# Performance work log

Hardware: AMD Instinct MI355X
Metric: run time of the kernel (lower is better)

## Reference

```python
import jax, jax.numpy as jnp
import numpy as np

NUM_HEADS = 16
EMBED_DIM = 2048
HEAD_DIM = EMBED_DIM // NUM_HEADS        # 128
LATENT_DIM = HEAD_DIM // 4               # 32
GROUPS = HEAD_DIM // LATENT_DIM          # 4 latent sub-heads per q head
B, T = 1, 2048


def setup_inputs() -> dict:
    key = jax.random.key(0)
    ks = jax.random.split(key, 7)
    s_in = 1.0 / np.sqrt(EMBED_DIM)
    x = jax.random.normal(ks[0], (B, T, EMBED_DIM), dtype=jnp.float32)
    # torch Linear weights: [out_features, in_features]
    Wq = jax.random.normal(ks[1], (EMBED_DIM, EMBED_DIM), dtype=jnp.float32) * s_in
    Wk = jax.random.normal(ks[2], (EMBED_DIM, EMBED_DIM), dtype=jnp.float32) * s_in
    Wv = jax.random.normal(ks[3], (EMBED_DIM, EMBED_DIM), dtype=jnp.float32) * s_in
    Wlk = jax.random.normal(ks[4], (NUM_HEADS * LATENT_DIM, EMBED_DIM), dtype=jnp.float32) * s_in
    Wlv = jax.random.normal(ks[5], (NUM_HEADS * LATENT_DIM, EMBED_DIM), dtype=jnp.float32) * s_in
    Wo = jax.random.normal(ks[6], (EMBED_DIM, EMBED_DIM), dtype=jnp.float32) * s_in
    return {"x": x, "Wq": Wq, "Wk": Wk, "Wv": Wv, "Wlk": Wlk, "Wlv": Wlv, "Wo": Wo}


def reference(x, Wq, Wk, Wv, Wlk, Wlv, Wo):
    Bv, Tv, C = x.shape
    # q: [B,T,H,G,Dl]  (each head's 128-dim q split into 4 latent sub-heads)
    q = (x @ Wq.T).reshape(Bv, Tv, NUM_HEADS, GROUPS, LATENT_DIM)
    # latent k/v: [B,T,H,Dl], shared across the G sub-heads of each q head
    lk = (x @ Wlk.T).reshape(Bv, Tv, NUM_HEADS, LATENT_DIM)
    lv = (x @ Wlv.T).reshape(Bv, Tv, NUM_HEADS, LATENT_DIM)
    # k_proj / v_proj outputs are computed but unused in the original forward.
    scale = 1.0 / np.sqrt(HEAD_DIM).astype(np.float32)
    # scores: [B,H,G,T,T]
    scores = jnp.einsum('bthgd,bshd->bhgts', q, lk) * scale
    probs = jax.nn.softmax(scores, axis=-1)
    out = jnp.einsum('bhgts,bshd->bthgd', probs, lv).reshape(Bv, Tv, C)
    return out @ Wo.T
```

## Files before the change

kernel.cpp:

```cpp
#include <hip/hip_runtime.h>
#include <hip/hip_bf16.h>

typedef __bf16 bf16;
typedef __bf16 bf16x4 __attribute__((ext_vector_type(4)));
typedef __bf16 bf16x8 __attribute__((ext_vector_type(8)));
typedef float  f32x4  __attribute__((ext_vector_type(4)));

#define AS1 __attribute__((address_space(1)))
#define AS3 __attribute__((address_space(3)))

__device__ __forceinline__ void gload_lds16(const bf16* g, bf16* l) {
    __builtin_amdgcn_global_load_lds((const AS1 void*)g, (AS3 void*)l, 16, 0, 0);
}

__device__ __forceinline__ void stage8_f32(const float* s, bf16* l) {
    float4 a = *(const float4*)s;
    float4 b = *(const float4*)(s + 4);
    bf16x8 o;
    o[0] = (bf16)a.x; o[1] = (bf16)a.y; o[2] = (bf16)a.z; o[3] = (bf16)a.w;
    o[4] = (bf16)b.x; o[5] = (bf16)b.y; o[6] = (bf16)b.z; o[7] = (bf16)b.w;
    *(bf16x8*)l = o;
}

template <bool AF32, bool BF32>
__device__ __forceinline__ void gemm_core64(
    const void* __restrict__ Av, const void* __restrict__ Bv,
    int m0, int n0, int K, f32x4 (&acc)[2][4],
    int wm, int r16, int q8)
{
    constexpr int LDA = AF32 ? 40 : 32;
    constexpr int LDB = BF32 ? 40 : 32;
    __shared__ __align__(16) bf16 As[2][128 * LDA];
    __shared__ __align__(16) bf16 Bs[2][64 * LDB];

    const int tid = threadIdx.x;
    const int i0 = tid, i1 = tid + 256;
    const int rA0 = i0 >> 2, rA1 = i1 >> 2;
    const int rB  = tid >> 2;
    const int c0  = (tid & 3) * 8;
    const size_t a0 = (size_t)(m0 + rA0) * K + c0;
    const size_t a1 = (size_t)(m0 + rA1) * K + c0;
    const size_t b0 = (size_t)(n0 + rB)  * K + c0;

    auto stage = [&](int buf, int k0) {
        if constexpr (AF32) {
            stage8_f32((const float*)Av + a0 + k0, &As[buf][rA0 * LDA + c0]);
            stage8_f32((const float*)Av + a1 + k0, &As[buf][rA1 * LDA + c0]);
        } else {
            gload_lds16((const bf16*)Av + a0 + k0, &As[buf][i0 * 8]);
            gload_lds16((const bf16*)Av + a1 + k0, &As[buf][i1 * 8]);
        }
        if constexpr (BF32) {
            stage8_f32((const float*)Bv + b0 + k0, &Bs[buf][rB * LDB + c0]);
        } else {
            gload_lds16((const bf16*)Bv + b0 + k0, &Bs[buf][tid * 8]);
        }
    };

    stage(0, 0);
    __syncthreads();

    int cur = 0;
    for (int k0 = 0; k0 < K; k0 += 32) {
        if (k0 + 32 < K) stage(cur ^ 1, k0 + 32);

        bf16x8 a[2], b[4];
#pragma unroll
        for (int r = 0; r < 2; ++r)
            a[r] = *(const bf16x8*)&As[cur][(wm + r * 16 + r16) * LDA + q8 * 8];
#pragma unroll
        for (int c = 0; c < 4; ++c)
            b[c] = *(const bf16x8*)&Bs[cur][(c * 16 + r16) * LDB + q8 * 8];
#pragma unroll
        for (int r = 0; r < 2; ++r)
#pragma unroll
            for (int c = 0; c < 4; ++c)
                acc[r][c] = __builtin_amdgcn_mfma_f32_16x16x32_bf16(a[r], b[c], acc[r][c], 0, 0, 0);

        asm volatile("s_waitcnt vmcnt(0) lgkmcnt(0)" ::: "memory");
        __builtin_amdgcn_s_barrier();
        __builtin_amdgcn_sched_barrier(0);
        cur ^= 1;
    }
}

__global__ __launch_bounds__(256) void cvt5(
    const float* __restrict__ s0, const float* __restrict__ s1,
    const float* __restrict__ s2, const float* __restrict__ s3,
    const float* __restrict__ s4,
    bf16* __restrict__ d0, bf16* __restrict__ d1, bf16* __restrict__ d2,
    bf16* __restrict__ d3, bf16* __restrict__ d4)
{
    const float* S[5] = {s0, s1, s2, s3, s4};
    bf16*        D[5] = {d0, d1, d2, d3, d4};
    const int    N[5] = {4194304, 4194304, 1048576, 1048576, 4194304};
    int y = blockIdx.y;
    int base = (blockIdx.x * 256 + threadIdx.x) * 8;
    if (base >= N[y]) return;
    stage8_f32(S[y] + base, D[y] + base);
}

template <bool F32>
__global__ __launch_bounds__(256) void proj_kernel_t(
    const void* __restrict__ x, const void* __restrict__ Wq,
    const void* __restrict__ Wlk, const void* __restrict__ Wlv,
    bf16* __restrict__ Q, bf16* __restrict__ LK, bf16* __restrict__ LVt)
{
    const int bx = blockIdx.x, by = blockIdx.y;
    const int tid = threadIdx.x, lane = tid & 63, wave = tid >> 6;
    const int wm = wave * 32;
    const int r16 = lane & 15, q8 = lane >> 4;
    f32x4 acc[2][4] = {};

    const void* Bv; int n0;
    if (bx < 32)      { Bv = Wq;  n0 = bx * 64; }
    else if (bx < 40) { Bv = Wlk; n0 = (bx - 32) * 64; }
    else              { Bv = Wlv; n0 = (bx - 40) * 64; }

    gemm_core64<F32, F32>(x, Bv, by * 128, n0, 2048, acc, wm, r16, q8);

    if (bx < 40) {
        bf16* C  = (bx < 32) ? Q : LK;
        int ldc  = (bx < 32) ? 2048 : 512;
        const float sc = (bx < 32) ? 0.08838834764831845f * 1.4426950408889634f : 1.0f;
#pragma unroll
        for (int r = 0; r < 2; ++r)
#pragma unroll
            for (int c = 0; c < 4; ++c)
#pragma unroll
                for (int i = 0; i < 4; ++i) {
                    int row = by * 128 + wm + r * 16 + q8 * 4 + i;
                    int col = n0 + c * 16 + r16;
                    C[(size_t)row * ldc + col] = (bf16)(acc[r][c][i] * sc);
                }
    } else {
#pragma unroll
        for (int r = 0; r < 2; ++r)
#pragma unroll
            for (int c = 0; c < 4; ++c) {
                int hd = n0 + c * 16 + r16;
                int tb = by * 128 + wm + r * 16 + q8 * 4;
                bf16x4 pk;
#pragma unroll
                for (int i = 0; i < 4; ++i) pk[i] = (bf16)acc[r][c][i];
                *(bf16x4*)&LVt[(size_t)hd * 2048 + tb] = pk;
            }
    }
}

template <bool BF32>
__global__ __launch_bounds__(256) void out_kernel_t(
    const bf16* __restrict__ A, const void* __restrict__ Wo, float* __restrict__ C)
{
    const int tid = threadIdx.x, lane = tid & 63, wave = tid >> 6;
    const int wm = wave * 32;
    const int r16 = lane & 15, q8 = lane >> 4;
    f32x4 acc[2][4] = {};
    gemm_core64<false, BF32>(A, Wo, blockIdx.y * 128, blockIdx.x * 64, 2048, acc, wm, r16, q8);
#pragma unroll
    for (int r = 0; r < 2; ++r)
#pragma unroll
        for (int c = 0; c < 4; ++c)
#pragma unroll
            for (int i = 0; i < 4; ++i) {
                int row = blockIdx.y * 128 + wm + r * 16 + q8 * 4 + i;
                int col = blockIdx.x * 64 + c * 16 + r16;
                C[(size_t)row * 2048 + col] = acc[r][c][i];
            }
}

__global__ __launch_bounds__(256, 4) void attn6(
    const bf16* __restrict__ Q, const bf16* __restrict__ LK,
    const bf16* __restrict__ LVt, bf16* __restrict__ O)
{
    __shared__ __align__(16) bf16 Ks[2][64 * 32];
    __shared__ __align__(16) bf16 Vs[2][32 * 64];
    __shared__ __align__(16) bf16 Ps[128 * 64];

    const int tid  = threadIdx.x;
    const int lane = tid & 63;
    const int w    = tid >> 6;
    const int r16  = lane & 15;
    const int q8   = lane >> 4;
    const int hg = blockIdx.y, h = hg >> 2, g = hg & 3;
    const int t0 = blockIdx.x * 128;

    bf16x8 qb[2];
#pragma unroll
    for (int p = 0; p < 2; ++p)
        qb[p] = *(const bf16x8*)(Q + (size_t)(t0 + w * 32 + p * 16 + r16) * 2048
                                 + h * 128 + g * 32 + q8 * 8);

    const int kr = tid >> 2;
    const int kq = (tid & 3) ^ ((tid >> 3) & 3);
    const bf16* kg = LK + (size_t)kr * 512 + h * 32 + kq * 8;
    const int vd = tid >> 3;
    const int vq = (tid & 7) ^ ((tid >> 3) & 7);
    const bf16* vg = LVt + (size_t)(h * 32 + vd) * 2048 + vq * 8;

    const int ksw = (r16 >> 1) & 3;
    const int vsw = r16 & 7;

    const int pk7 = r16 & 7;
    const int ph  = q8 >> 1;
    const int plo = (q8 & 1) * 4;
    const int pb0 = ((w * 2 + 0) * 16 + r16) * 64;
    const int pb1 = ((w * 2 + 1) * 16 + r16) * 64;

    bf16x8 ones;
#pragma unroll
    for (int j = 0; j < 8; ++j) ones[j] = (bf16)1.0f;

    f32x4 o_acc[2][2] = {};
    f32x4 l_acc[2] = {};
    const f32x4 z = {0.f, 0.f, 0.f, 0.f};

    gload_lds16(kg, &Ks[0][tid * 8]);
    gload_lds16(vg, &Vs[0][tid * 8]);
    __syncthreads();

    int cur = 0;
    for (int sb = 0; sb < 2048; sb += 64) {
        if (sb + 64 < 2048) {
            gload_lds16(kg + (size_t)(sb + 64) * 512, &Ks[cur ^ 1][tid * 8]);
            gload_lds16(vg + (sb + 64),               &Vs[cur ^ 1][tid * 8]);
        }
        const bf16* ks = Ks[cur];
        const bf16* vs = Vs[cur];

        bf16x8 kb[4], vb[2][2];
#pragma unroll
        for (int c = 0; c < 4; ++c)
            kb[c] = *(const bf16x8*)&ks[(c * 16 + r16) * 32 + (q8 ^ ksw) * 8];
#pragma unroll
        for (int kk = 0; kk < 2; ++kk)
#pragma unroll
            for (int ct = 0; ct < 2; ++ct)
                vb[kk][ct] = *(const bf16x8*)&vs[(ct * 16 + r16) * 64
                                                 + (((kk * 4 + q8) ^ vsw) * 8)];

#pragma unroll
        for (int p = 0; p < 2; ++p) {
            const int pbase = p ? pb1 : pb0;
            f32x4 s[4];
            __builtin_amdgcn_s_setprio(1);
#pragma unroll
            for (int c = 0; c < 4; ++c)
                s[c] = __builtin_amdgcn_mfma_f32_16x16x32_bf16(kb[c], qb[p], z, 0, 0, 0);
            __builtin_amdgcn_s_setprio(0);
#pragma unroll
            for (int c = 0; c < 4; ++c) {
                bf16x4 pkv;
#pragma unroll
                for (int i = 0; i < 4; ++i) pkv[i] = (bf16)exp2f(s[c][i]);
                *(bf16x4*)&Ps[pbase + ((c * 2 + ph) ^ pk7) * 8 + plo] = pkv;
            }
        }

        __builtin_amdgcn_s_setprio(1);
#pragma unroll
        for (int p = 0; p < 2; ++p) {
            const int pbase = p ? pb1 : pb0;
#pragma unroll
            for (int kk = 0; kk < 2; ++kk) {
                bf16x8 ap = *(const bf16x8*)&Ps[pbase + ((kk * 4 + q8) ^ pk7) * 8];
#pragma unroll
                for (int ct = 0; ct < 2; ++ct)
                    o_acc[p][ct] = __builtin_amdgcn_mfma_f32_16x16x32_bf16(ap, vb[kk][ct], o_acc[p][ct], 0, 0, 0);
                l_acc[p] = __builtin_amdgcn_mfma_f32_16x16x32_bf16(ap, ones, l_acc[p], 0, 0, 0);
            }
        }
        __builtin_amdgcn_s_setprio(0);

        asm volatile("s_waitcnt vmcnt(0) lgkmcnt(0)" ::: "memory");
        __builtin_amdgcn_s_barrier();
        __builtin_amdgcn_sched_barrier(0);
        cur ^= 1;
    }

#pragma unroll
    for (int p = 0; p < 2; ++p)
#pragma unroll
        for (int i = 0; i < 4; ++i) {
            float inv = 1.0f / l_acc[p][i];
            int t = t0 + w * 32 + p * 16 + q8 * 4 + i;
#pragma unroll
            for (int ct = 0; ct < 2; ++ct) {
                int d = ct * 16 + r16;
                O[(size_t)t * 2048 + h * 128 + g * 32 + d] = (bf16)(o_acc[p][ct][i] * inv);
            }
        }
}

extern "C" void kernel_launch(void* const* d_in, const int* in_sizes, int n_in,
                              void* d_out, int out_size, void* d_ws, size_t ws_size,
                              hipStream_t stream) {
    const float* x   = (const float*)d_in[0];
    const float* Wq  = (const float*)d_in[1];
    const float* Wlk = (const float*)d_in[4];
    const float* Wlv = (const float*)d_in[5];
    const float* Wo  = (const float*)d_in[6];
    float* out = (float*)d_out;

    const size_t M4 = 4194304, M1 = 1048576;
    const size_t need_fast = (M1 + M1 + M4 + M4 + M1 + M1) * 2;

    if (ws_size >= need_fast) {
        bf16* xb   = (bf16*)d_out;
        bf16* Wqb  = xb + M4;
        bf16* p    = (bf16*)d_ws;
        bf16* Wlkb = p; p += M1;
        bf16* Wlvb = p; p += M1;
        bf16* Wob  = p; p += M4;
        bf16* Qp   = p; p += M4;
        bf16* LKp  = p; p += M1;
        bf16* LVt  = p;
        bf16* ATT  = Qp;

        cvt5<<<dim3(2048, 5), 256, 0, stream>>>(x, Wq, Wlk, Wlv, Wo,
                                                xb, Wqb, Wlkb, Wlvb, Wob);
        proj_kernel_t<false><<<dim3(48, 16), 256, 0, stream>>>(xb, Wqb, Wlkb, Wlvb,
                                                               Qp, LKp, LVt);
        attn6<<<dim3(16, 64), 256, 0, stream>>>(Qp, LKp, LVt, ATT);
        out_kernel_t<false><<<dim3(32, 16), 256, 0, stream>>>(ATT, Wob, out);
    } else {
        bf16* Qp  = (bf16*)d_ws;
        bf16* LKp = Qp + M4;
        bf16* LVt = LKp + M1;
        bf16* ATT = Qp;

        proj_kernel_t<true><<<dim3(48, 16), 256, 0, stream>>>(x, Wq, Wlk, Wlv,
                                                              Qp, LKp, LVt);
        attn6<<<dim3(16, 64), 256, 0, stream>>>(Qp, LKp, LVt, ATT);
        out_kernel_t<true><<<dim3(32, 16), 256, 0, stream>>>(ATT, Wo, out);
    }
}
```

Before: 284.6 us.

## Drop separate fp32-to-bf16 conversion pass; convert in GEMM staging, triple-buffer attention

The separate conversion kernel is removed, so the projection and output GEMMs now read fp32 inputs and weights directly. They convert to bf16 in registers while staging into XOR-swizzled LDS tiles with a K-step of 64, and prefetch the next tile into registers during the MFMA work. The attention kernel moves from double to triple buffering of K/V tiles with a partial vmcnt wait, so loads can run two iterations ahead. This avoids a full extra read and write of all weights and x, at the cost of heavier per-block global traffic (fp32 reads of weights repeated across blocks), more register pressure, and larger LDS use.

```diff
diff --git a/kernel.cpp b/kernel.cpp
--- a/kernel.cpp
+++ b/kernel.cpp
@@ -13,111 +13,96 @@
     __builtin_amdgcn_global_load_lds((const AS1 void*)g, (AS3 void*)l, 16, 0, 0);
 }
 
-__device__ __forceinline__ void stage8_f32(const float* s, bf16* l) {
-    float4 a = *(const float4*)s;
-    float4 b = *(const float4*)(s + 4);
+__device__ __forceinline__ bf16x8 pack8(const float4 a, const float4 b) {
     bf16x8 o;
     o[0] = (bf16)a.x; o[1] = (bf16)a.y; o[2] = (bf16)a.z; o[3] = (bf16)a.w;
     o[4] = (bf16)b.x; o[5] = (bf16)b.y; o[6] = (bf16)b.z; o[7] = (bf16)b.w;
-    *(bf16x8*)l = o;
-}
-
-template <bool AF32, bool BF32>
-__device__ __forceinline__ void gemm_core64(
-    const void* __restrict__ Av, const void* __restrict__ Bv,
-    int m0, int n0, int K, f32x4 (&acc)[2][4],
-    int wm, int r16, int q8)
-{
-    constexpr int LDA = AF32 ? 40 : 32;
-    constexpr int LDB = BF32 ? 40 : 32;
-    __shared__ __align__(16) bf16 As[2][128 * LDA];
-    __shared__ __align__(16) bf16 Bs[2][64 * LDB];
-
-    const int tid = threadIdx.x;
-    const int i0 = tid, i1 = tid + 256;
-    const int rA0 = i0 >> 2, rA1 = i1 >> 2;
-    const int rB  = tid >> 2;
-    const int c0  = (tid & 3) * 8;
-    const size_t a0 = (size_t)(m0 + rA0) * K + c0;
-    const size_t a1 = (size_t)(m0 + rA1) * K + c0;
-    const size_t b0 = (size_t)(n0 + rB)  * K + c0;
-
-    auto stage = [&](int buf, int k0) {
-        if constexpr (AF32) {
-            stage8_f32((const float*)Av + a0 + k0, &As[buf][rA0 * LDA + c0]);
-            stage8_f32((const float*)Av + a1 + k0, &As[buf][rA1 * LDA + c0]);
-        } else {
-            gload_lds16((const bf16*)Av + a0 + k0, &As[buf][i0 * 8]);
-            gload_lds16((const bf16*)Av + a1 + k0, &As[buf][i1 * 8]);
-        }
-        if constexpr (BF32) {
-            stage8_f32((const float*)Bv + b0 + k0, &Bs[buf][rB * LDB + c0]);
-        } else {
-            gload_lds16((const bf16*)Bv + b0 + k0, &Bs[buf][tid * 8]);
-        }
-    };
-
-    stage(0, 0);
-    __syncthreads();
-
-    int cur = 0;
-    for (int k0 = 0; k0 < K; k0 += 32) {
-        if (k0 + 32 < K) stage(cur ^ 1, k0 + 32);
-
-        bf16x8 a[2], b[4];
-#pragma unroll
-        for (int r = 0; r < 2; ++r)
-            a[r] = *(const bf16x8*)&As[cur][(wm + r * 16 + r16) * LDA + q8 * 8];
-#pragma unroll
-        for (int c = 0; c < 4; ++c)
-            b[c] = *(const bf16x8*)&Bs[cur][(c * 16 + r16) * LDB + q8 * 8];
-#pragma unroll
-        for (int r = 0; r < 2; ++r)
-#pragma unroll
-            for (int c = 0; c < 4; ++c)
-                acc[r][c] = __builtin_amdgcn_mfma_f32_16x16x32_bf16(a[r], b[c], acc[r][c], 0, 0, 0);
-
-        asm volatile("s_waitcnt vmcnt(0) lgkmcnt(0)" ::: "memory");
-        __builtin_amdgcn_s_barrier();
-        __builtin_amdgcn_sched_barrier(0);
-        cur ^= 1;
-    }
-}
-
-__global__ __launch_bounds__(256) void cvt5(
-    const float* __restrict__ s0, const float* __restrict__ s1,
-    const float* __restrict__ s2, const float* __restrict__ s3,
-    const float* __restrict__ s4,
-    bf16* __restrict__ d0, bf16* __restrict__ d1, bf16* __restrict__ d2,
-    bf16* __restrict__ d3, bf16* __restrict__ d4)
-{
-    const float* S[5] = {s0, s1, s2, s3, s4};
-    bf16*        D[5] = {d0, d1, d2, d3, d4};
-    const int    N[5] = {4194304, 4194304, 1048576, 1048576, 4194304};
-    int y = blockIdx.y;
-    int base = (blockIdx.x * 256 + threadIdx.x) * 8;
-    if (base >= N[y]) return;
-    stage8_f32(S[y] + base, D[y] + base);
-}
-
-template <bool F32>
-__global__ __launch_bounds__(256) void proj_kernel_t(
-    const void* __restrict__ x, const void* __restrict__ Wq,
-    const void* __restrict__ Wlk, const void* __restrict__ Wlv,
+    return o;
+}
+
+__global__ __launch_bounds__(256, 3) void proj9(
+    const float* __restrict__ x, const float* __restrict__ Wq,
+    const float* __restrict__ Wlk, const float* __restrict__ Wlv,
     bf16* __restrict__ Q, bf16* __restrict__ LK, bf16* __restrict__ LVt)
 {
+    __shared__ __align__(16) bf16 As[2][128 * 64];
+    __shared__ __align__(16) bf16 Bs[2][64 * 64];
+
     const int bx = blockIdx.x, by = blockIdx.y;
     const int tid = threadIdx.x, lane = tid & 63, wave = tid >> 6;
     const int wm = wave * 32;
     const int r16 = lane & 15, q8 = lane >> 4;
+    const int k7 = r16 & 7;
+
+    const float* Bp; int n0;
+    if (bx < 32)      { Bp = Wq;  n0 = bx * 64; }
+    else if (bx < 40) { Bp = Wlk; n0 = (bx - 32) * 64; }
+    else              { Bp = Wlv; n0 = (bx - 40) * 64; }
+
+    const int s = tid >> 3, c = tid & 7;
+    const int gqe = (c ^ (s & 7)) * 8;
+    const float* aSrc = x  + (size_t)(by * 128 + s) * 2048 + gqe;
+    const float* bSrc = Bp + (size_t)(n0 + s) * 2048 + gqe;
+
     f32x4 acc[2][4] = {};
-
-    const void* Bv; int n0;
-    if (bx < 32)      { Bv = Wq;  n0 = bx * 64; }
-    else if (bx < 40) { Bv = Wlk; n0 = (bx - 32) * 64; }
-    else              { Bv = Wlv; n0 = (bx - 40) * 64; }
-
-    gemm_core64<F32, F32>(x, Bv, by * 128, n0, 2048, acc, wm, r16, q8);
+    float4 ra[4][2], rb[2][2];
+
+    auto loads = [&](int kt) {
+#pragma unroll
+        for (int j = 0; j < 4; ++j) {
+            const float* p = aSrc + (size_t)j * 32 * 2048 + kt;
+            ra[j][0] = *(const float4*)p;
+            ra[j][1] = *(const float4*)(p + 4);
+        }
+#pragma unroll
+        for (int j = 0; j < 2; ++j) {
+            const float* p = bSrc + (size_t)j * 32 * 2048 + kt;
+            rb[j][0] = *(const float4*)p;
+            rb[j][1] = *(const float4*)(p + 4);
+        }
+    };
+    auto writes = [&](int buf) {
+#pragma unroll
+        for (int j = 0; j < 4; ++j)
+            *(bf16x8*)&As[buf][(j * 32 + s) * 64 + c * 8] = pack8(ra[j][0], ra[j][1]);
+#pragma unroll
+        for (int j = 0; j < 2; ++j)
+            *(bf16x8*)&Bs[buf][(j * 32 + s) * 64 + c * 8] = pack8(rb[j][0], rb[j][1]);
+    };
+
+    loads(0); writes(0);
+    __syncthreads();
+
+    int cur = 0;
+    for (int kt = 0; kt < 2048; kt += 64) {
+        const bool pf = (kt + 64 < 2048);
+        if (pf) loads(kt + 64);
+
+        bf16x8 a[2][2], b[4][2];
+#pragma unroll
+        for (int r = 0; r < 2; ++r)
+#pragma unroll
+            for (int kc = 0; kc < 2; ++kc)
+                a[r][kc] = *(const bf16x8*)&As[cur][(wm + r * 16 + r16) * 64
+                                                   + ((kc * 4 + q8) ^ k7) * 8];
+#pragma unroll
+        for (int cc = 0; cc < 4; ++cc)
+#pragma unroll
+            for (int kc = 0; kc < 2; ++kc)
+                b[cc][kc] = *(const bf16x8*)&Bs[cur][(cc * 16 + r16) * 64
+                                                    + ((kc * 4 + q8) ^ k7) * 8];
+#pragma unroll
+        for (int kc = 0; kc < 2; ++kc)
+#pragma unroll
+            for (int r = 0; r < 2; ++r)
+#pragma unroll
+                for (int cc = 0; cc < 4; ++cc)
+                    acc[r][cc] = __builtin_amdgcn_mfma_f32_16x16x32_bf16(a[r][kc], b[cc][kc], acc[r][cc], 0, 0, 0);
+
+        if (pf) writes(cur ^ 1);
+        __syncthreads();
+        cur ^= 1;
+    }
 
     if (bx < 40) {
         bf16* C  = (bx < 32) ? Q : LK;
@@ -126,55 +111,119 @@
 #pragma unroll
         for (int r = 0; r < 2; ++r)
 #pragma unroll
-            for (int c = 0; c < 4; ++c)
+            for (int cc = 0; cc < 4; ++cc)
 #pragma unroll
                 for (int i = 0; i < 4; ++i) {
                     int row = by * 128 + wm + r * 16 + q8 * 4 + i;
-                    int col = n0 + c * 16 + r16;
-                    C[(size_t)row * ldc + col] = (bf16)(acc[r][c][i] * sc);
+                    int col = n0 + cc * 16 + r16;
+                    C[(size_t)row * ldc + col] = (bf16)(acc[r][cc][i] * sc);
                 }
     } else {
 #pragma unroll
         for (int r = 0; r < 2; ++r)
 #pragma unroll
-            for (int c = 0; c < 4; ++c) {
-                int hd = n0 + c * 16 + r16;
+            for (int cc = 0; cc < 4; ++cc) {
+                int hd = n0 + cc * 16 + r16;
                 int tb = by * 128 + wm + r * 16 + q8 * 4;
                 bf16x4 pk;
 #pragma unroll
-                for (int i = 0; i < 4; ++i) pk[i] = (bf16)acc[r][c][i];
+                for (int i = 0; i < 4; ++i) pk[i] = (bf16)acc[r][cc][i];
                 *(bf16x4*)&LVt[(size_t)hd * 2048 + tb] = pk;
             }
     }
 }
 
-template <bool BF32>
-__global__ __launch_bounds__(256) void out_kernel_t(
-    const bf16* __restrict__ A, const void* __restrict__ Wo, float* __restrict__ C)
+__global__ __launch_bounds__(256, 3) void out9(
+    const bf16* __restrict__ A, const float* __restrict__ Wo, float* __restrict__ C)
 {
+    __shared__ __align__(16) bf16 As[2][128 * 64];
+    __shared__ __align__(16) bf16 Bs[2][64 * 64];
+
     const int tid = threadIdx.x, lane = tid & 63, wave = tid >> 6;
     const int wm = wave * 32;
     const int r16 = lane & 15, q8 = lane >> 4;
+    const int k7 = r16 & 7;
+    const int m0 = blockIdx.y * 128, n0 = blockIdx.x * 64;
+
+    const int s = tid >> 3, c = tid & 7;
+    const int gqe = (c ^ (s & 7)) * 8;
+    const bf16*  aSrc = A  + (size_t)(m0 + s) * 2048 + gqe;
+    const float* bSrc = Wo + (size_t)(n0 + s) * 2048 + gqe;
+
     f32x4 acc[2][4] = {};
-    gemm_core64<false, BF32>(A, Wo, blockIdx.y * 128, blockIdx.x * 64, 2048, acc, wm, r16, q8);
+    float4 rb[2][2];
+
+    auto stageA = [&](int buf, int kt) {
+#pragma unroll
+        for (int j = 0; j < 4; ++j)
+            gload_lds16(aSrc + (size_t)j * 32 * 2048 + kt, &As[buf][(j * 256 + tid) * 8]);
+    };
+    auto loadB = [&](int kt) {
+#pragma unroll
+        for (int j = 0; j < 2; ++j) {
+            const float* p = bSrc + (size_t)j * 32 * 2048 + kt;
+            rb[j][0] = *(const float4*)p;
+            rb[j][1] = *(const float4*)(p + 4);
+        }
+    };
+    auto writeB = [&](int buf) {
+#pragma unroll
+        for (int j = 0; j < 2; ++j)
+            *(bf16x8*)&Bs[buf][(j * 32 + s) * 64 + c * 8] = pack8(rb[j][0], rb[j][1]);
+    };
+
+    stageA(0, 0); loadB(0); writeB(0);
+    __syncthreads();
+
+    int cur = 0;
+    for (int kt = 0; kt < 2048; kt += 64) {
+        const bool pf = (kt + 64 < 2048);
+        if (pf) { stageA(cur ^ 1, kt + 64); loadB(kt + 64); }
+
+        bf16x8 a[2][2], b[4][2];
+#pragma unroll
+        for (int r = 0; r < 2; ++r)
+#pragma unroll
+            for (int kc = 0; kc < 2; ++kc)
+                a[r][kc] = *(const bf16x8*)&As[cur][(wm + r * 16 + r16) * 64
+                                                   + ((kc * 4 + q8) ^ k7) * 8];
+#pragma unroll
+        for (int cc = 0; cc < 4; ++cc)
+#pragma unroll
+            for (int kc = 0; kc < 2; ++kc)
+                b[cc][kc] = *(const bf16x8*)&Bs[cur][(cc * 16 + r16) * 64
+                                                    + ((kc * 4 + q8) ^ k7) * 8];
+#pragma unroll
+        for (int kc = 0; kc < 2; ++kc)
+#pragma unroll
+            for (int r = 0; r < 2; ++r)
+#pragma unroll
+                for (int cc = 0; cc < 4; ++cc)
+                    acc[r][cc] = __builtin_amdgcn_mfma_f32_16x16x32_bf16(a[r][kc], b[cc][kc], acc[r][cc], 0, 0, 0);
+
+        if (pf) writeB(cur ^ 1);
+        __syncthreads();
+        cur ^= 1;
+    }
+
 #pragma unroll
     for (int r = 0; r < 2; ++r)
 #pragma unroll
-        for (int c = 0; c < 4; ++c)
+        for (int cc = 0; cc < 4; ++cc)
 #pragma unroll
             for (int i = 0; i < 4; ++i) {
-                int row = blockIdx.y * 128 + wm + r * 16 + q8 * 4 + i;
-                int col = blockIdx.x * 64 + c * 16 + r16;
-                C[(size_t)row * 2048 + col] = acc[r][c][i];
-            }
-}
-
-__global__ __launch_bounds__(256, 4) void attn6(
+                int row = m0 + wm + r * 16 + q8 * 4 + i;
+                int col = n0 + cc * 16 + r16;
+                C[(size_t)row * 2048 + col] = acc[r][cc][i];
+            }
+}
+
+__global__ __launch_bounds__(256, 4) void attn7(
     const bf16* __restrict__ Q, const bf16* __restrict__ LK,
     const bf16* __restrict__ LVt, bf16* __restrict__ O)
 {
-    __shared__ __align__(16) bf16 Ks[2][64 * 32];
-    __shared__ __align__(16) bf16 Vs[2][32 * 64];
+    __shared__ __align__(16) bf16 Ks[3][64 * 32];
+    __shared__ __align__(16) bf16 Vs[3][32 * 64];
     __shared__ __align__(16) bf16 Ps[128 * 64];
 
     const int tid  = threadIdx.x;
@@ -215,23 +264,26 @@
     f32x4 l_acc[2] = {};
     const f32x4 z = {0.f, 0.f, 0.f, 0.f};
 
-    gload_lds16(kg, &Ks[0][tid * 8]);
-    gload_lds16(vg, &Vs[0][tid * 8]);
+    gload_lds16(kg,                 &Ks[0][tid * 8]);
+    gload_lds16(vg,                 &Vs[0][tid * 8]);
+    gload_lds16(kg + (size_t)64 * 512, &Ks[1][tid * 8]);
+    gload_lds16(vg + 64,               &Vs[1][tid * 8]);
     __syncthreads();
 
-    int cur = 0;
+    int cur = 0, stg = 2;
     for (int sb = 0; sb < 2048; sb += 64) {
-        if (sb + 64 < 2048) {
-            gload_lds16(kg + (size_t)(sb + 64) * 512, &Ks[cur ^ 1][tid * 8]);
-            gload_lds16(vg + (sb + 64),               &Vs[cur ^ 1][tid * 8]);
+        const bool pf = (sb + 128 < 2048);
+        if (pf) {
+            gload_lds16(kg + (size_t)(sb + 128) * 512, &Ks[stg][tid * 8]);
+            gload_lds16(vg + (sb + 128),               &Vs[stg][tid * 8]);
         }
         const bf16* ks = Ks[cur];
         const bf16* vs = Vs[cur];
 
         bf16x8 kb[4], vb[2][2];
 #pragma unroll
-        for (int c = 0; c < 4; ++c)
-            kb[c] = *(const bf16x8*)&ks[(c * 16 + r16) * 32 + (q8 ^ ksw) * 8];
+        for (int cc = 0; cc < 4; ++cc)
+            kb[cc] = *(const bf16x8*)&ks[(cc * 16 + r16) * 32 + (q8 ^ ksw) * 8];
 #pragma unroll
         for (int kk = 0; kk < 2; ++kk)
 #pragma unroll
@@ -242,18 +294,18 @@
 #pragma unroll
         for (int p = 0; p < 2; ++p) {
             const int pbase = p ? pb1 : pb0;
-            f32x4 s[4];
+            f32x4 sv[4];
             __builtin_amdgcn_s_setprio(1);
 #pragma unroll
-            for (int c = 0; c < 4; ++c)
-                s[c] = __builtin_amdgcn_mfma_f32_16x16x32_bf16(kb[c], qb[p], z, 0, 0, 0);
+            for (int cc = 0; cc < 4; ++cc)
+                sv[cc] = __builtin_amdgcn_mfma_f32_16x16x32_bf16(kb[cc], qb[p], z, 0, 0, 0);
             __builtin_amdgcn_s_setprio(0);
 #pragma unroll
-            for (int c = 0; c < 4; ++c) {
+            for (int cc = 0; cc < 4; ++cc) {
                 bf16x4 pkv;
 #pragma unroll
-                for (int i = 0; i < 4; ++i) pkv[i] = (bf16)exp2f(s[c][i]);
-                *(bf16x4*)&Ps[pbase + ((c * 2 + ph) ^ pk7) * 8 + plo] = pkv;
+                for (int i = 0; i < 4; ++i) pkv[i] = (bf16)exp2f(sv[cc][i]);
+                *(bf16x4*)&Ps[pbase + ((cc * 2 + ph) ^ pk7) * 8 + plo] = pkv;
             }
         }
 
@@ -272,10 +324,12 @@
         }
         __builtin_amdgcn_s_setprio(0);
 
-        asm volatile("s_waitcnt vmcnt(0) lgkmcnt(0)" ::: "memory");
+        if (pf) asm volatile("s_waitcnt vmcnt(2) lgkmcnt(0)" ::: "memory");
+        else    asm volatile("s_waitcnt vmcnt(0) lgkmcnt(0)" ::: "memory");
         __builtin_amdgcn_s_barrier();
         __builtin_amdgcn_sched_barrier(0);
-        cur ^= 1;
+        cur = (cur == 2) ? 0 : cur + 1;
+        stg = (stg == 2) ? 0 : stg + 1;
     }
 
 #pragma unroll
@@ -303,35 +357,12 @@
     float* out = (float*)d_out;
 
     const size_t M4 = 4194304, M1 = 1048576;
-    const size_t need_fast = (M1 + M1 + M4 + M4 + M1 + M1) * 2;
-
-    if (ws_size >= need_fast) {
-        bf16* xb   = (bf16*)d_out;
-        bf16* Wqb  = xb + M4;
-        bf16* p    = (bf16*)d_ws;
-        bf16* Wlkb = p; p += M1;
-        bf16* Wlvb = p; p += M1;
-        bf16* Wob  = p; p += M4;
-        bf16* Qp   = p; p += M4;
-        bf16* LKp  = p; p += M1;
-        bf16* LVt  = p;
-        bf16* ATT  = Qp;
-
-        cvt5<<<dim3(2048, 5), 256, 0, stream>>>(x, Wq, Wlk, Wlv, Wo,
-                                                xb, Wqb, Wlkb, Wlvb, Wob);
-        proj_kernel_t<false><<<dim3(48, 16), 256, 0, stream>>>(xb, Wqb, Wlkb, Wlvb,
-                                                               Qp, LKp, LVt);
-        attn6<<<dim3(16, 64), 256, 0, stream>>>(Qp, LKp, LVt, ATT);
-        out_kernel_t<false><<<dim3(32, 16), 256, 0, stream>>>(ATT, Wob, out);
-    } else {
-        bf16* Qp  = (bf16*)d_ws;
-        bf16* LKp = Qp + M4;
-        bf16* LVt = LKp + M1;
-        bf16* ATT = Qp;
-
-        proj_kernel_t<true><<<dim3(48, 16), 256, 0, stream>>>(x, Wq, Wlk, Wlv,
-                                                              Qp, LKp, LVt);
-        attn6<<<dim3(16, 64), 256, 0, stream>>>(Qp, LKp, LVt, ATT);
-        out_kernel_t<true><<<dim3(32, 16), 256, 0, stream>>>(ATT, Wo, out);
-    }
-}
+    bf16* Qp  = (bf16*)d_ws;
+    bf16* LKp = Qp + M4;
+    bf16* LVt = LKp + M1;
+    bf16* ATT = Qp;
+
+    proj9<<<dim3(48, 16), 256, 0, stream>>>(x, Wq, Wlk, Wlv, Qp, LKp, LVt);
+    attn7<<<dim3(16, 64), 256, 0, stream>>>(Qp, LKp, LVt, ATT);
+    out9<<<dim3(32, 16), 256, 0, stream>>>(ATT, Wo, out);
+}
```

Result: slower. 294.8 us (+3.6%).

## Use K=64 swizzled GEMM tiles, triple-buffer attention, fuse Wo conversion into attention

Applied to the files above, without the earlier changes.

The shared GEMM core now stages 64-wide K tiles through direct global-to-LDS loads with an XOR swizzle, halving the number of barriers per K loop. The attention kernel moves from double to triple buffering of K/V tiles and waits with a partial vmcnt so prefetches two steps ahead stay in flight. The Wo fp32-to-bf16 conversion is moved out of the separate convert kernel into the tail of the attention kernel so it overlaps with attention work. The fp32 fallback path for small workspaces is removed, which drops support for that case, and LDS use per block grows.

```diff
diff --git a/kernel.cpp b/kernel.cpp
--- a/kernel.cpp
+++ b/kernel.cpp
@@ -22,60 +22,57 @@
     *(bf16x8*)l = o;
 }
 
-template <bool AF32, bool BF32>
-__device__ __forceinline__ void gemm_core64(
-    const void* __restrict__ Av, const void* __restrict__ Bv,
+__device__ __forceinline__ void gemm_core64_k64(
+    const bf16* __restrict__ A, const bf16* __restrict__ B,
     int m0, int n0, int K, f32x4 (&acc)[2][4],
     int wm, int r16, int q8)
 {
-    constexpr int LDA = AF32 ? 40 : 32;
-    constexpr int LDB = BF32 ? 40 : 32;
-    __shared__ __align__(16) bf16 As[2][128 * LDA];
-    __shared__ __align__(16) bf16 Bs[2][64 * LDB];
-
-    const int tid = threadIdx.x;
-    const int i0 = tid, i1 = tid + 256;
-    const int rA0 = i0 >> 2, rA1 = i1 >> 2;
-    const int rB  = tid >> 2;
-    const int c0  = (tid & 3) * 8;
-    const size_t a0 = (size_t)(m0 + rA0) * K + c0;
-    const size_t a1 = (size_t)(m0 + rA1) * K + c0;
-    const size_t b0 = (size_t)(n0 + rB)  * K + c0;
-
-    auto stage = [&](int buf, int k0) {
-        if constexpr (AF32) {
-            stage8_f32((const float*)Av + a0 + k0, &As[buf][rA0 * LDA + c0]);
-            stage8_f32((const float*)Av + a1 + k0, &As[buf][rA1 * LDA + c0]);
-        } else {
-            gload_lds16((const bf16*)Av + a0 + k0, &As[buf][i0 * 8]);
-            gload_lds16((const bf16*)Av + a1 + k0, &As[buf][i1 * 8]);
-        }
-        if constexpr (BF32) {
-            stage8_f32((const float*)Bv + b0 + k0, &Bs[buf][rB * LDB + c0]);
-        } else {
-            gload_lds16((const bf16*)Bv + b0 + k0, &Bs[buf][tid * 8]);
-        }
+    __shared__ __align__(16) bf16 As[2][128 * 64];
+    __shared__ __align__(16) bf16 Bs[2][64 * 64];
+
+    const int tid  = threadIdx.x;
+    const int arow = tid >> 3;
+    const int acol = ((tid & 7) ^ ((tid >> 3) & 7)) * 8;
+    const int k7   = r16 & 7;
+
+    auto stage = [&](int buf, int kt) {
+#pragma unroll
+        for (int j = 0; j < 4; ++j)
+            gload_lds16(A + (size_t)(m0 + j * 32 + arow) * K + kt + acol,
+                        &As[buf][(j * 256 + tid) * 8]);
+#pragma unroll
+        for (int j = 0; j < 2; ++j)
+            gload_lds16(B + (size_t)(n0 + j * 32 + arow) * K + kt + acol,
+                        &Bs[buf][(j * 256 + tid) * 8]);
     };
 
     stage(0, 0);
     __syncthreads();
 
     int cur = 0;
-    for (int k0 = 0; k0 < K; k0 += 32) {
-        if (k0 + 32 < K) stage(cur ^ 1, k0 + 32);
-
-        bf16x8 a[2], b[4];
+    for (int kt = 0; kt < K; kt += 64) {
+        if (kt + 64 < K) stage(cur ^ 1, kt + 64);
+
+        bf16x8 a[2][2], b[4][2];
 #pragma unroll
         for (int r = 0; r < 2; ++r)
-            a[r] = *(const bf16x8*)&As[cur][(wm + r * 16 + r16) * LDA + q8 * 8];
+#pragma unroll
+            for (int kc = 0; kc < 2; ++kc)
+                a[r][kc] = *(const bf16x8*)&As[cur][(wm + r * 16 + r16) * 64
+                                                   + ((kc * 4 + q8) ^ k7) * 8];
 #pragma unroll
         for (int c = 0; c < 4; ++c)
-            b[c] = *(const bf16x8*)&Bs[cur][(c * 16 + r16) * LDB + q8 * 8];
-#pragma unroll
-        for (int r = 0; r < 2; ++r)
-#pragma unroll
-            for (int c = 0; c < 4; ++c)
-                acc[r][c] = __builtin_amdgcn_mfma_f32_16x16x32_bf16(a[r], b[c], acc[r][c], 0, 0, 0);
+#pragma unroll
+            for (int kc = 0; kc < 2; ++kc)
+                b[c][kc] = *(const bf16x8*)&Bs[cur][(c * 16 + r16) * 64
+                                                   + ((kc * 4 + q8) ^ k7) * 8];
+#pragma unroll
+        for (int kc = 0; kc < 2; ++kc)
+#pragma unroll
+            for (int r = 0; r < 2; ++r)
+#pragma unroll
+                for (int c = 0; c < 4; ++c)
+                    acc[r][c] = __builtin_amdgcn_mfma_f32_16x16x32_bf16(a[r][kc], b[c][kc], acc[r][c], 0, 0, 0);
 
         asm volatile("s_waitcnt vmcnt(0) lgkmcnt(0)" ::: "memory");
         __builtin_amdgcn_s_barrier();
@@ -84,26 +81,24 @@
     }
 }
 
-__global__ __launch_bounds__(256) void cvt5(
+__global__ __launch_bounds__(256) void cvt4(
     const float* __restrict__ s0, const float* __restrict__ s1,
     const float* __restrict__ s2, const float* __restrict__ s3,
-    const float* __restrict__ s4,
     bf16* __restrict__ d0, bf16* __restrict__ d1, bf16* __restrict__ d2,
-    bf16* __restrict__ d3, bf16* __restrict__ d4)
-{
-    const float* S[5] = {s0, s1, s2, s3, s4};
-    bf16*        D[5] = {d0, d1, d2, d3, d4};
-    const int    N[5] = {4194304, 4194304, 1048576, 1048576, 4194304};
+    bf16* __restrict__ d3)
+{
+    const float* S[4] = {s0, s1, s2, s3};
+    bf16*        D[4] = {d0, d1, d2, d3};
+    const int    N[4] = {4194304, 4194304, 1048576, 1048576};
     int y = blockIdx.y;
     int base = (blockIdx.x * 256 + threadIdx.x) * 8;
     if (base >= N[y]) return;
     stage8_f32(S[y] + base, D[y] + base);
 }
 
-template <bool F32>
-__global__ __launch_bounds__(256) void proj_kernel_t(
-    const void* __restrict__ x, const void* __restrict__ Wq,
-    const void* __restrict__ Wlk, const void* __restrict__ Wlv,
+__global__ __launch_bounds__(256) void proj_k64(
+    const bf16* __restrict__ x, const bf16* __restrict__ Wq,
+    const bf16* __restrict__ Wlk, const bf16* __restrict__ Wlv,
     bf16* __restrict__ Q, bf16* __restrict__ LK, bf16* __restrict__ LVt)
 {
     const int bx = blockIdx.x, by = blockIdx.y;
@@ -112,12 +107,12 @@
     const int r16 = lane & 15, q8 = lane >> 4;
     f32x4 acc[2][4] = {};
 
-    const void* Bv; int n0;
+    const bf16* Bv; int n0;
     if (bx < 32)      { Bv = Wq;  n0 = bx * 64; }
     else if (bx < 40) { Bv = Wlk; n0 = (bx - 32) * 64; }
     else              { Bv = Wlv; n0 = (bx - 40) * 64; }
 
-    gemm_core64<F32, F32>(x, Bv, by * 128, n0, 2048, acc, wm, r16, q8);
+    gemm_core64_k64(x, Bv, by * 128, n0, 2048, acc, wm, r16, q8);
 
     if (bx < 40) {
         bf16* C  = (bx < 32) ? Q : LK;
@@ -148,15 +143,14 @@
     }
 }
 
-template <bool BF32>
-__global__ __launch_bounds__(256) void out_kernel_t(
-    const bf16* __restrict__ A, const void* __restrict__ Wo, float* __restrict__ C)
+__global__ __launch_bounds__(256) void out_k64(
+    const bf16* __restrict__ A, const bf16* __restrict__ Wob, float* __restrict__ C)
 {
     const int tid = threadIdx.x, lane = tid & 63, wave = tid >> 6;
     const int wm = wave * 32;
     const int r16 = lane & 15, q8 = lane >> 4;
     f32x4 acc[2][4] = {};
-    gemm_core64<false, BF32>(A, Wo, blockIdx.y * 128, blockIdx.x * 64, 2048, acc, wm, r16, q8);
+    gemm_core64_k64(A, Wob, blockIdx.y * 128, blockIdx.x * 64, 2048, acc, wm, r16, q8);
 #pragma unroll
     for (int r = 0; r < 2; ++r)
 #pragma unroll
@@ -169,12 +163,13 @@
             }
 }
 
-__global__ __launch_bounds__(256, 4) void attn6(
+__global__ __launch_bounds__(256, 4) void attn7(
     const bf16* __restrict__ Q, const bf16* __restrict__ LK,
-    const bf16* __restrict__ LVt, bf16* __restrict__ O)
-{
-    __shared__ __align__(16) bf16 Ks[2][64 * 32];
-    __shared__ __align__(16) bf16 Vs[2][32 * 64];
+    const bf16* __restrict__ LVt, bf16* __restrict__ O,
+    const float* __restrict__ Wo, bf16* __restrict__ Wob)
+{
+    __shared__ __align__(16) bf16 Ks[3][64 * 32];
+    __shared__ __align__(16) bf16 Vs[3][32 * 64];
     __shared__ __align__(16) bf16 Ps[128 * 64];
 
     const int tid  = threadIdx.x;
@@ -215,23 +210,26 @@
     f32x4 l_acc[2] = {};
     const f32x4 z = {0.f, 0.f, 0.f, 0.f};
 
-    gload_lds16(kg, &Ks[0][tid * 8]);
-    gload_lds16(vg, &Vs[0][tid * 8]);
+    gload_lds16(kg,                 &Ks[0][tid * 8]);
+    gload_lds16(vg,                 &Vs[0][tid * 8]);
+    gload_lds16(kg + (size_t)64 * 512, &Ks[1][tid * 8]);
+    gload_lds16(vg + 64,               &Vs[1][tid * 8]);
     __syncthreads();
 
-    int cur = 0;
+    int cur = 0, stg = 2;
     for (int sb = 0; sb < 2048; sb += 64) {
-        if (sb + 64 < 2048) {
-            gload_lds16(kg + (size_t)(sb + 64) * 512, &Ks[cur ^ 1][tid * 8]);
-            gload_lds16(vg + (sb + 64),               &Vs[cur ^ 1][tid * 8]);
+        const bool pf = (sb + 128 < 2048);
+        if (pf) {
+            gload_lds16(kg + (size_t)(sb + 128) * 512, &Ks[stg][tid * 8]);
+            gload_lds16(vg + (sb + 128),               &Vs[stg][tid * 8]);
         }
         const bf16* ks = Ks[cur];
         const bf16* vs = Vs[cur];
 
         bf16x8 kb[4], vb[2][2];
 #pragma unroll
-        for (int c = 0; c < 4; ++c)
-            kb[c] = *(const bf16x8*)&ks[(c * 16 + r16) * 32 + (q8 ^ ksw) * 8];
+        for (int cc = 0; cc < 4; ++cc)
+            kb[cc] = *(const bf16x8*)&ks[(cc * 16 + r16) * 32 + (q8 ^ ksw) * 8];
 #pragma unroll
         for (int kk = 0; kk < 2; ++kk)
 #pragma unroll
@@ -242,18 +240,18 @@
 #pragma unroll
         for (int p = 0; p < 2; ++p) {
             const int pbase = p ? pb1 : pb0;
-            f32x4 s[4];
+            f32x4 sv[4];
             __builtin_amdgcn_s_setprio(1);
 #pragma unroll
-            for (int c = 0; c < 4; ++c)
-                s[c] = __builtin_amdgcn_mfma_f32_16x16x32_bf16(kb[c], qb[p], z, 0, 0, 0);
+            for (int cc = 0; cc < 4; ++cc)
+                sv[cc] = __builtin_amdgcn_mfma_f32_16x16x32_bf16(kb[cc], qb[p], z, 0, 0, 0);
             __builtin_amdgcn_s_setprio(0);
 #pragma unroll
-            for (int c = 0; c < 4; ++c) {
+            for (int cc = 0; cc < 4; ++cc) {
                 bf16x4 pkv;
 #pragma unroll
-                for (int i = 0; i < 4; ++i) pkv[i] = (bf16)exp2f(s[c][i]);
-                *(bf16x4*)&Ps[pbase + ((c * 2 + ph) ^ pk7) * 8 + plo] = pkv;
+                for (int i = 0; i < 4; ++i) pkv[i] = (bf16)exp2f(sv[cc][i]);
+                *(bf16x4*)&Ps[pbase + ((cc * 2 + ph) ^ pk7) * 8 + plo] = pkv;
             }
         }
 
@@ -272,10 +270,12 @@
         }
         __builtin_amdgcn_s_setprio(0);
 
-        asm volatile("s_waitcnt vmcnt(0) lgkmcnt(0)" ::: "memory");
+        if (pf) asm volatile("s_waitcnt vmcnt(2) lgkmcnt(0)" ::: "memory");
+        else    asm volatile("s_waitcnt vmcnt(0) lgkmcnt(0)" ::: "memory");
         __builtin_amdgcn_s_barrier();
         __builtin_amdgcn_sched_barrier(0);
-        cur ^= 1;
+        cur = (cur == 2) ? 0 : cur + 1;
+        stg = (stg == 2) ? 0 : stg + 1;
     }
 
 #pragma unroll
@@ -290,6 +290,15 @@
                 O[(size_t)t * 2048 + h * 128 + g * 32 + d] = (bf16)(o_acc[p][ct][i] * inv);
             }
         }
+
+    {
+        const int bid = blockIdx.y * 16 + blockIdx.x;
+#pragma unroll
+        for (int it = 0; it < 2; ++it) {
+            size_t off = (size_t)bid * 4096 + (size_t)it * 2048 + (size_t)tid * 8;
+            stage8_f32(Wo + off, Wob + off);
+        }
+    }
 }
 
 extern "C" void kernel_launch(void* const* d_in, const int* in_sizes, int n_in,
@@ -303,35 +312,21 @@
     float* out = (float*)d_out;
 
     const size_t M4 = 4194304, M1 = 1048576;
-    const size_t need_fast = (M1 + M1 + M4 + M4 + M1 + M1) * 2;
-
-    if (ws_size >= need_fast) {
-        bf16* xb   = (bf16*)d_out;
-        bf16* Wqb  = xb + M4;
-        bf16* p    = (bf16*)d_ws;
-        bf16* Wlkb = p; p += M1;
-        bf16* Wlvb = p; p += M1;
-        bf16* Wob  = p; p += M4;
-        bf16* Qp   = p; p += M4;
-        bf16* LKp  = p; p += M1;
-        bf16* LVt  = p;
-        bf16* ATT  = Qp;
-
-        cvt5<<<dim3(2048, 5), 256, 0, stream>>>(x, Wq, Wlk, Wlv, Wo,
-                                                xb, Wqb, Wlkb, Wlvb, Wob);
-        proj_kernel_t<false><<<dim3(48, 16), 256, 0, stream>>>(xb, Wqb, Wlkb, Wlvb,
-                                                               Qp, LKp, LVt);
-        attn6<<<dim3(16, 64), 256, 0, stream>>>(Qp, LKp, LVt, ATT);
-        out_kernel_t<false><<<dim3(32, 16), 256, 0, stream>>>(ATT, Wob, out);
-    } else {
-        bf16* Qp  = (bf16*)d_ws;
-        bf16* LKp = Qp + M4;
-        bf16* LVt = LKp + M1;
-        bf16* ATT = Qp;
-
-        proj_kernel_t<true><<<dim3(48, 16), 256, 0, stream>>>(x, Wq, Wlk, Wlv,
-                                                              Qp, LKp, LVt);
-        attn6<<<dim3(16, 64), 256, 0, stream>>>(Qp, LKp, LVt, ATT);
-        out_kernel_t<true><<<dim3(32, 16), 256, 0, stream>>>(ATT, Wo, out);
-    }
-}
+    bf16* xb   = (bf16*)d_out;
+    bf16* Wqb  = xb + M4;
+    bf16* p    = (bf16*)d_ws;
+    bf16* Wlkb = p; p += M1;
+    bf16* Wlvb = p; p += M1;
+    bf16* Wob  = p; p += M4;
+    bf16* Qp   = p; p += M4;
+    bf16* LKp  = p; p += M1;
+    bf16* LVt  = p;
+    bf16* ATT  = Qp;
+
+    cvt4<<<dim3(2048, 4), 256, 0, stream>>>(x, Wq, Wlk, Wlv,
+                                            xb, Wqb, Wlkb, Wlvb);
+    proj_k64<<<dim3(48, 16), 256, 0, stream>>>(xb, Wqb, Wlkb, Wlvb,
+                                               Qp, LKp, LVt);
+    attn7<<<dim3(16, 64), 256, 0, stream>>>(Qp, LKp, LVt, ATT, Wo, Wob);
+    out_k64<<<dim3(32, 16), 256, 0, stream>>>(ATT, Wob, out);
+}
```

Result: faster. 266.0 us (-6.6%).
